# Optimization experiments

Hardware: AMD Instinct MI355X
Metric: run time of the kernel (lower is better)

Reference implementation:

```python
import jax, jax.numpy as jnp
import numpy as np

D_MODEL = 1024
NUM_HEADS = 16
D_FF = 4096
SEQ = 2048
BATCH = 2
THETA = 10000.0
EPS = 1e-5


def _param(key, shape, fan_in, fan_out):
    std = 2.0 / (fan_in + fan_out) ** 0.5
    return std * jax.random.truncated_normal(key, -3.0, 3.0, shape, dtype=jnp.float32)


def setup_inputs() -> dict:
    key = jax.random.key(0)
    ks = jax.random.split(key, 8)
    d, h, f = D_MODEL, NUM_HEADS, D_FF
    return {
        'x': jax.random.normal(ks[0], (BATCH, SEQ, d), dtype=jnp.float32),
        'token_positions': jnp.arange(SEQ, dtype=jnp.int32),
        'wq': _param(ks[1], (d, d), d, d),
        'wk': _param(ks[2], (d, d), d, d),
        'wv': _param(ks[3], (d, d), d, d),
        'wo': _param(ks[4], (d, d), d, d),
        'ln1_w': jnp.ones((d,), jnp.float32),
        'ln2_w': jnp.ones((d,), jnp.float32),
        'w1': _param(ks[5], (f, d), d, f),
        'w2': _param(ks[6], (d, f), f, d),
        'w3': _param(ks[7], (f, d), d, f),
    }


def rmsnorm(x, w):
    x32 = x.astype(jnp.float32)
    rms = jnp.sqrt(jnp.mean(x32 * x32, axis=-1, keepdims=True) + EPS)
    return ((x32 / rms) * w).astype(x.dtype)


def apply_rope(x, cos, sin):
    # x: [b, h, s, d_k]; cos/sin: [s, d_k//2] -> broadcast as [1,1,s,d_k//2]
    xe, xo = x[..., ::2], x[..., 1::2]
    c = cos[None, None, :, :]
    s = sin[None, None, :, :]
    re = xe * c - xo * s
    ro = xe * s + xo * c
    return jnp.stack((re, ro), axis=-1).reshape(x.shape)


def block_forward(x, token_positions, wq, wk, wv, wo, ln1_w, ln2_w, w1, w2, w3):
    b, s, d = x.shape
    h = NUM_HEADS
    dk = d // h
    # RoPE tables at token positions
    inv_freq = 1.0 / (THETA ** (jnp.arange(0, dk // 2, dtype=jnp.float32) * 2.0 / dk))
    freqs = token_positions.astype(jnp.float32)[:, None] * inv_freq[None, :]  # [s, dk/2]
    cos, sin = jnp.cos(freqs), jnp.sin(freqs)

    # --- attention sublayer (pre-norm) ---
    xn = rmsnorm(x, ln1_w)
    q = jnp.einsum('bsd,ed->bse', xn, wq).reshape(b, s, h, dk).transpose(0, 2, 1, 3)
    k = jnp.einsum('bsd,ed->bse', xn, wk).reshape(b, s, h, dk).transpose(0, 2, 1, 3)
    v = jnp.einsum('bsd,ed->bse', xn, wv).reshape(b, s, h, dk).transpose(0, 2, 1, 3)
    q = apply_rope(q, cos, sin)
    k = apply_rope(k, cos, sin)
    scores = jnp.einsum('bhqd,bhkd->bhqk', q, k) / jnp.sqrt(jnp.float32(dk))
    causal = jnp.tril(jnp.ones((s, s), dtype=bool))
    scores = jnp.where(causal[None, None], scores, -jnp.inf)
    attn = jax.nn.softmax(scores, axis=-1)
    o = jnp.einsum('bhqk,bhkd->bhqd', attn, v)
    o = o.transpose(0, 2, 1, 3).reshape(b, s, d)
    x = x + jnp.einsum('bse,de->bsd', o, wo)

    # --- SwiGLU sublayer (pre-norm) ---
    xn = rmsnorm(x, ln2_w)
    x1 = jnp.einsum('bsd,fd->bsf', xn, w1)
    x3 = jnp.einsum('bsd,fd->bsf', xn, w3)
    gated = (x1 * jax.nn.sigmoid(x1)) * x3
    return x + jnp.einsum('bsf,df->bsd', gated, w2)


def reference(x, token_positions, wq, wk, wv, wo, ln1_w, ln2_w, w1, w2, w3):
    return block_forward(x, token_positions, wq, wk, wv, wo, ln1_w, ln2_w, w1, w2, w3)
```

## Files before the change

### kernel.cpp

```cpp
#include <hip/hip_runtime.h>
#include <hip/hip_bf16.h>

typedef __attribute__((ext_vector_type(4))) float f32x4;
typedef __attribute__((ext_vector_type(8))) short bf16x8;
typedef unsigned short u16;
typedef unsigned int u32;
typedef __attribute__((ext_vector_type(4))) u16 u16x4;

#define DEV static __device__ __forceinline__

constexpr int Bb = 2, Ss = 2048, Dd = 1024, Hh = 16, DKk = 64;
constexpr int Mm = Bb * Ss;

DEV float bf2f(u16 u) { union { u32 i; float f; } v; v.i = (u32)u << 16; return v.f; }
DEV u16 f2bf(float f) {
  union { float f; u32 i; } v; v.f = f;
  u32 r = v.i + 0x7FFFu + ((v.i >> 16) & 1u);
  return (u16)(r >> 16);
}

DEV void gload_lds16(const u16* g, u16* l) {
  __builtin_amdgcn_global_load_lds((const __attribute__((address_space(1))) u32*)g,
                                   (__attribute__((address_space(3))) u32*)l, 16, 0, 0);
}

DEV int swz16(int o) {
  return o ^ (((o >> 8) & 1) << 6) ^ (((o >> 9) & 1) << 5);
}

__global__ void k_cvt_all(const float* __restrict__ wq, const float* __restrict__ wk,
                          const float* __restrict__ wv, const float* __restrict__ wo,
                          const float* __restrict__ w1, const float* __restrict__ w2,
                          const float* __restrict__ w3,
                          u16* __restrict__ wqkv, u16* __restrict__ wob,
                          u16* __restrict__ w13, u16* __restrict__ w2b) {
  int i = (blockIdx.x * 256 + threadIdx.x) * 4;
  int seg = i >> 20;
  const float* src; u16* dst;
  if (seg == 0)      { src = wq + i;             dst = wqkv + i; }
  else if (seg == 1) { src = wk + (i - (1<<20)); dst = wqkv + i; }
  else if (seg == 2) { src = wv + (i - (2<<20)); dst = wqkv + i; }
  else if (seg == 3) { src = wo + (i - (3<<20)); dst = wob  + (i - (3<<20)); }
  else if (seg < 8)  { src = w1 + (i - (4<<20)); dst = w13  + (i - (4<<20)); }
  else if (seg < 12) { src = w2 + (i - (8<<20)); dst = w2b  + (i - (8<<20)); }
  else               { src = w3 + (i - (12<<20)); dst = w13 + (4<<20) + (i - (12<<20)); }
  float4 v = *(const float4*)src;
  u16x4 o = { f2bf(v.x), f2bf(v.y), f2bf(v.z), f2bf(v.w) };
  *(u16x4*)dst = o;
}

__global__ __launch_bounds__(256) void k_rmsnorm(const float* __restrict__ x,
                                                 const float* __restrict__ w,
                                                 u16* __restrict__ out) {
  int row = blockIdx.x;
  int t = threadIdx.x;
  float4 v = ((const float4*)(x + (long)row * Dd))[t];
  float ss = v.x * v.x + v.y * v.y + v.z * v.z + v.w * v.w;
#pragma unroll
  for (int m = 32; m; m >>= 1) ss += __shfl_xor(ss, m, 64);
  __shared__ float red[4];
  if ((t & 63) == 0) red[t >> 6] = ss;
  __syncthreads();
  float tot = red[0] + red[1] + red[2] + red[3];
  float r = rsqrtf(tot * (1.0f / Dd) + 1e-5f);
  float4 wv = ((const float4*)w)[t];
  u16x4 o = { f2bf(v.x * r * wv.x), f2bf(v.y * r * wv.y),
              f2bf(v.z * r * wv.z), f2bf(v.w * r * wv.w) };
  ((u16x4*)(out + (long)row * Dd))[t] = o;
}

__global__ void k_rope(u16* __restrict__ q, u16* __restrict__ k, const int* __restrict__ tp) {
  int idx = blockIdx.x * 256 + threadIdx.x;
  if (idx >= Bb * Ss * Hh * 32) return;
  int p = idx & 31;
  int h = (idx >> 5) & 15;
  int row = idx >> 9;
  int s = row & (Ss - 1);
  float pos = (float)tp[s];
  float invf = __expf(-(float)p * (2.0f / DKk) * 9.2103403719761836f);
  float fr = pos * invf;
  float sn, cs;
  sincosf(fr, &sn, &cs);
  long base = (long)row * Dd + h * DKk + 2 * p;
  float xe = bf2f(q[base]), xo = bf2f(q[base + 1]);
  q[base]     = f2bf((xe * cs - xo * sn) * 0.125f);
  q[base + 1] = f2bf((xe * sn + xo * cs) * 0.125f);
  xe = bf2f(k[base]); xo = bf2f(k[base + 1]);
  k[base]     = f2bf(xe * cs - xo * sn);
  k[base + 1] = f2bf(xe * sn + xo * cs);
}

__global__ void k_gate(u16* __restrict__ x1, const u16* __restrict__ x3, int n) {
  int i = (blockIdx.x * 256 + threadIdx.x) * 4;
  if (i >= n) return;
  u16x4 a = *(u16x4*)(x1 + i);
  u16x4 b = *(const u16x4*)(x3 + i);
#pragma unroll
  for (int j = 0; j < 4; j++) {
    float v = bf2f(a[j]);
    float g = v / (1.0f + __expf(-v)) * bf2f(b[j]);
    a[j] = f2bf(g);
  }
  *(u16x4*)(x1 + i) = a;
}

__global__ void k_addout(const float* __restrict__ p0, const float* __restrict__ p1,
                         const float* __restrict__ x2, float* __restrict__ out) {
  int i = (blockIdx.x * 256 + threadIdx.x) * 4;
  float4 a = *(const float4*)(p0 + i);
  float4 b = *(const float4*)(p1 + i);
  float4 c = *(const float4*)(x2 + i);
  float4 o = { a.x + b.x + c.x, a.y + b.y + c.y, a.z + b.z + c.z, a.w + b.w + c.w };
  *(float4*)(out + i) = o;
}

template <int OM, bool RES>
__global__ __launch_bounds__(256) void k_gemm(const u16* __restrict__ A,
                                              const u16* __restrict__ Bm,
                                              void* __restrict__ Cout,
                                              const float* __restrict__ Rres,
                                              int N, int Kl, int Kstr) {
  __shared__ u16 Abuf[128 * 32];
  __shared__ u16 Bbuf[128 * 32];
  const int tid = threadIdx.x;
  const int wid = tid >> 6, lane = tid & 63;
  const int wm = wid >> 1, wn = wid & 1;
  const int lq = lane >> 4, ll = lane & 15;
  const int lin = blockIdx.y * gridDim.x + blockIdx.x;
  const int c = lin & 7, j = lin >> 3;
  const int ncc = gridDim.x >> 2;
  const int bxc = (c % ncc) * 4 + (j & 3);
  const int byc = (c / ncc) * 8 + (j >> 2);
  const int m0 = byc * 128, n0 = bxc * 128;

  const u16* Ap = A + (long)blockIdx.z * Kl;
  const u16* Bp = Bm + (long)blockIdx.z * Kl;

  f32x4 acc[4][4] = {};

  const int srow = tid >> 2;
  const int scol = (tid & 3) * 8;
  const long aoff = (long)(m0 + srow) * Kstr + scol;
  const long boff = (long)(n0 + srow) * Kstr + scol;
  u16* aldsw = Abuf + wid * 512;
  u16* bldsw = Bbuf + wid * 512;

  for (int k0 = 0; k0 < Kl; k0 += 32) {
    __syncthreads();
    gload_lds16(Ap + aoff + k0, aldsw);
    gload_lds16(Ap + aoff + (long)64 * Kstr + k0, aldsw + 2048);
    gload_lds16(Bp + boff + k0, bldsw);
    gload_lds16(Bp + boff + (long)64 * Kstr + k0, bldsw + 2048);
    __syncthreads();
    bf16x8 af[4], bfr[4];
#pragma unroll
    for (int i = 0; i < 4; i++)
      af[i] = *(const bf16x8*)&Abuf[(wm * 64 + i * 16 + ll) * 32 + lq * 8];
#pragma unroll
    for (int j2 = 0; j2 < 4; j2++)
      bfr[j2] = *(const bf16x8*)&Bbuf[(wn * 64 + j2 * 16 + ll) * 32 + lq * 8];
#pragma unroll
    for (int i = 0; i < 4; i++)
#pragma unroll
      for (int j2 = 0; j2 < 4; j2++)
        acc[i][j2] = __builtin_amdgcn_mfma_f32_16x16x32_bf16(af[i], bfr[j2], acc[i][j2], 0, 0, 0);
  }

  float* fout = (float*)Cout + (long)blockIdx.z * Mm * (long)N;
#pragma unroll
  for (int i = 0; i < 4; i++) {
    const int rowb = m0 + wm * 64 + i * 16 + lq * 4;
#pragma unroll
    for (int j2 = 0; j2 < 4; j2++) {
      const int col = n0 + wn * 64 + j2 * 16 + ll;
#pragma unroll
      for (int r = 0; r < 4; r++) {
        int rr = rowb + r;
        float v = acc[i][j2][r];
        if (RES) v += Rres[(long)rr * N + col];
        if (OM == 1) {
          fout[(long)rr * N + col] = v;
        } else {
          ((u16*)Cout)[(long)rr * N + col] = f2bf(v);
        }
      }
    }
  }
}

#define STG_A(d, h, kt)                                                         \
  { gload_lds16(A + aoff[0] + (long)(h) * 128 * K + (kt) * 64, &sA[d][h][dst0]); \
    gload_lds16(A + aoff[1] + (long)(h) * 128 * K + (kt) * 64, &sA[d][h][dst1]); }
#define STG_B(d, h, kt)                                                         \
  { gload_lds16(Bm + boff[0] + (long)(h) * 128 * K + (kt) * 64, &sB[d][h][dst0]); \
    gload_lds16(Bm + boff[1] + (long)(h) * 128 * K + (kt) * 64, &sB[d][h][dst1]); }

#define PHASE(q, d, DOB, WVN, ...)                                              \
  {                                                                             \
    bf16x8 af_[2][2];                                                           \
    _Pragma("unroll") for (int s_ = 0; s_ < 2; s_++)                            \
    _Pragma("unroll") for (int kk_ = 0; kk_ < 2; kk_++) {                       \
      int ms_ = (q) * 4 + wm * 2 + s_;                                          \
      int lo_ = ((ms_ & 7) * 16 + ll) * 128 + kk_ * 64 + lq * 16;               \
      af_[s_][kk_] = *(const bf16x8*)((const char*)sA[d][ms_ >> 3] + swz16(lo_)); \
    }                                                                           \
    if (DOB) {                                                                  \
      _Pragma("unroll") for (int ns_ = 0; ns_ < 4; ns_++)                       \
      _Pragma("unroll") for (int kk_ = 0; kk_ < 2; kk_++) {                     \
        int rl_ = wn * 64 + ns_ * 16 + ll;                                      \
        int lo_ = (rl_ & 127) * 128 + kk_ * 64 + lq * 16;                       \
        bfr[ns_][kk_] = *(const bf16x8*)((const char*)sB[d][rl_ >> 7] + swz16(lo_)); \
      }                                                                         \
    }                                                                           \
    __VA_ARGS__;                                                                \
    __builtin_amdgcn_s_barrier();                                               \
    asm volatile("s_waitcnt lgkmcnt(0)" ::: "memory");                          \
    __builtin_amdgcn_sched_barrier(0);                                          \
    __builtin_amdgcn_s_setprio(1);                                              \
    _Pragma("unroll") for (int s_ = 0; s_ < 2; s_++)                            \
    _Pragma("unroll") for (int ns_ = 0; ns_ < 4; ns_++)                         \
    _Pragma("unroll") for (int kk_ = 0; kk_ < 2; kk_++)                         \
      acc[q][s_][ns_] = __builtin_amdgcn_mfma_f32_16x16x32_bf16(                \
          af_[s_][kk_], bfr[ns_][kk_], acc[q][s_][ns_], 0, 0, 0);               \
    __builtin_amdgcn_s_setprio(0);                                              \
    { int wv_ = (WVN);                                                          \
      if (wv_ == 6) { asm volatile("s_waitcnt vmcnt(6)" ::: "memory"); }        \
      else if (wv_ == 0) { asm volatile("s_waitcnt vmcnt(0)" ::: "memory"); } } \
    __builtin_amdgcn_s_barrier();                                               \
  }

template <int OM, int CW, int CH>
__global__ __launch_bounds__(512) void k_gemm8(const u16* __restrict__ A,
                                               const u16* __restrict__ Bm,
                                               void* __restrict__ Cout,
                                               int N, int K) {
  __shared__ u16 sA[2][2][8192];
  __shared__ u16 sB[2][2][8192];
  const int gx = gridDim.x;
  const int lin = blockIdx.y * gx + blockIdx.x;
  const int c = lin & 7, j = lin >> 3;
  const int ncc = gx / CW;
  const int bx = (c % ncc) * CW + j % CW;
  const int by = (c / ncc) * CH + j / CW;
  const long m0 = (long)by * 256, n0 = (long)bx * 256;
  const int tid = threadIdx.x;
  const int wid = tid >> 6, lane = tid & 63;
  const int wm = wid >> 2, wn = wid & 3;
  const int lq = lane >> 4, ll = lane & 15;

  long aoff[2], boff[2];
#pragma unroll
  for (int j2 = 0; j2 < 2; j2++) {
    int off = j2 * 8192 + wid * 1024 + lane * 16;
    int lo = swz16(off);
    int r = lo >> 7, cc = (lo & 127) >> 1;
    aoff[j2] = (m0 + r) * K + cc;
    boff[j2] = (n0 + r) * K + cc;
  }
  const int dst0 = wid * 512;
  const int dst1 = 4096 + wid * 512;

  f32x4 acc[4][2][4] = {};
  bf16x8 bfr[4][2];

  const int NT = K >> 6;
  const int NI = NT >> 1;

  STG_A(0, 0, 0); STG_A(0, 1, 0); STG_B(0, 0, 0); STG_B(0, 1, 0);
  STG_B(1, 0, 1); STG_B(1, 1, 1); STG_A(1, 0, 1);
  asm volatile("s_waitcnt vmcnt(6)" ::: "memory");
  __builtin_amdgcn_s_barrier();

  for (int it = 0; it < NI; it++) {
    const int t = 2 * it;
    const bool full = (t + 2 < NT);
    PHASE(0, 0, true,  -1,            STG_A(1, 1, t + 1))
    PHASE(1, 0, false, -1,            if (full) STG_B(0, 0, t + 2))
    PHASE(2, 0, false, -1,            if (full) STG_B(0, 1, t + 2))
    PHASE(3, 0, false, full ? 6 : 0,  if (full) STG_A(0, 0, t + 2))
    PHASE(0, 1, true,  -1,            if (full) STG_A(0, 1, t + 2))
    PHASE(1, 1, false, -1,            if (full) STG_B(1, 0, t + 3))
    PHASE(2, 1, false, -1,            if (full) STG_B(1, 1, t + 3))
    PHASE(3, 1, false, full ? 6 : -1, if (full) STG_A(1, 0, t + 3))
  }

#pragma unroll
  for (int q = 0; q < 4; q++)
#pragma unroll
    for (int s = 0; s < 2; s++) {
      const long row0 = m0 + (q * 4 + wm * 2 + s) * 16 + lq * 4;
#pragma unroll
      for (int ns = 0; ns < 4; ns++) {
        const long col = n0 + wn * 64 + ns * 16 + ll;
#pragma unroll
        for (int r = 0; r < 4; r++) {
          float v = acc[q][s][ns][r];
          long rr = row0 + r;
          if (OM == 3) {
            if (col < 2048) {
              ((u16*)Cout)[(col >> 10) * (long)(Mm * 1024) + rr * 1024 + (col & 1023)] = f2bf(v);
            } else {
              int d = col & 63, hh = ((int)col >> 6) & 15;
              int b2 = (int)rr >> 11, s2 = (int)rr & (Ss - 1);
              ((u16*)Cout)[(long)(2 * Mm * 1024) + ((long)((b2 * Hh + hh) * DKk + d)) * Ss + s2] = f2bf(v);
            }
          } else {
            ((u16*)Cout)[(col >> 12) * ((long)Mm * 4096) + rr * 4096 + (col & 4095)] = f2bf(v);
          }
        }
      }
    }
}

constexpr int PPAD = 80;

DEV void attn_tile(const u16* __restrict__ Kc, const u16* __restrict__ Vc,
                   u16* __restrict__ myP, const bf16x8* qf, f32x4* accO,
                   float* mrow, float* lrow, int qloc, bool diag, int lq, int ll) {
  f32x4 sacc[4] = {};
#pragma unroll
  for (int fn = 0; fn < 4; fn++)
#pragma unroll
    for (int ks = 0; ks < 2; ks++) {
      bf16x8 kf = *(const bf16x8*)&Kc[(fn * 16 + ll) * 64 + (((ks * 4 + lq) ^ (ll & 7)) * 8)];
      sacc[fn] = __builtin_amdgcn_mfma_f32_16x16x32_bf16(qf[ks], kf, sacc[fn], 0, 0, 0);
    }
  float sv[4][4], pmax[4];
#pragma unroll
  for (int r = 0; r < 4; r++) pmax[r] = -1e30f;
#pragma unroll
  for (int fn = 0; fn < 4; fn++) {
    int kc = fn * 16 + ll;
#pragma unroll
    for (int r = 0; r < 4; r++) {
      float v = sacc[fn][r];
      if (diag && kc > qloc + r) v = -1e30f;
      sv[fn][r] = v;
      pmax[r] = fmaxf(pmax[r], v);
    }
  }
#pragma unroll
  for (int r = 0; r < 4; r++) {
#pragma unroll
    for (int m = 1; m < 16; m <<= 1) pmax[r] = fmaxf(pmax[r], __shfl_xor(pmax[r], m, 64));
  }
  float alpha[4], rsum[4];
#pragma unroll
  for (int r = 0; r < 4; r++) {
    float mnew = fmaxf(mrow[r], pmax[r]);
    alpha[r] = __expf(mrow[r] - mnew);
    mrow[r] = mnew;
    rsum[r] = 0.f;
  }
#pragma unroll
  for (int fn = 0; fn < 4; fn++) {
#pragma unroll
    for (int r = 0; r < 4; r++) {
      float p = __expf(sv[fn][r] - mrow[r]);
      rsum[r] += p;
      myP[(lq * 4 + r) * PPAD + fn * 16 + ll] = f2bf(p);
    }
  }
#pragma unroll
  for (int r = 0; r < 4; r++) {
#pragma unroll
    for (int m = 1; m < 16; m <<= 1) rsum[r] += __shfl_xor(rsum[r], m, 64);
    lrow[r] = lrow[r] * alpha[r] + rsum[r];
  }
#pragma unroll
  for (int fn = 0; fn < 4; fn++)
#pragma unroll
    for (int r = 0; r < 4; r++) accO[fn][r] *= alpha[r];
  bf16x8 pa[2];
#pragma unroll
  for (int ks = 0; ks < 2; ks++)
    pa[ks] = *(const bf16x8*)&myP[ll * PPAD + ks * 32 + lq * 8];
#pragma unroll
  for (int fn = 0; fn < 4; fn++)
#pragma unroll
    for (int ks = 0; ks < 2; ks++) {
      bf16x8 vf = *(const bf16x8*)&Vc[(fn * 16 + ll) * 64 + (((ks * 4 + lq) ^ (ll & 7)) * 8)];
      accO[fn] = __builtin_amdgcn_mfma_f32_16x16x32_bf16(pa[ks], vf, accO[fn], 0, 0, 0);
    }
}

__global__ __launch_bounds__(256) void k_attn(const u16* __restrict__ Q,
                                              const u16* __restrict__ Kb,
                                              const u16* __restrict__ VT,
                                              u16* __restrict__ O) {
  __shared__ u16 Kt[2][64 * 64];
  __shared__ u16 Vt[2][64 * 64];
  __shared__ u16 P[4][16 * PPAD];
  const int pair = blockIdx.x;
  const int bh = blockIdx.y;
  const int b = bh >> 4, h = bh & 15;
  const int tid = threadIdx.x;
  const int wid = tid >> 6, lane = tid & 63;
  const int lq = lane >> 4, ll = lane & 15;
  const int qtA = pair, qtB = 31 - pair;
  const int qr0A = qtA * 64 + wid * 16;
  const int qr0B = qtB * 64 + wid * 16;
  const int qloc = wid * 16 + lq * 4;
  const long qkbase = ((long)b * Ss) * Dd + h * DKk;
  const long vbase  = ((long)(b * Hh + h) * DKk) * Ss;
  const int nk = 32 - pair;

  const int slot0 = wid * 64 + lane;
  const int r0 = slot0 >> 3, c0 = (slot0 & 7) ^ (r0 & 7);
  const int slot1 = 256 + slot0;
  const int r1 = slot1 >> 3, c1 = (slot1 & 7) ^ (r1 & 7);
  const int ldsb0 = (wid * 64) * 8;
  const int ldsb1 = (256 + wid * 64) * 8;

  bf16x8 qfA[2], qfB[2];
#pragma unroll
  for (int ks = 0; ks < 2; ks++) {
    qfA[ks] = *(const bf16x8*)&Q[qkbase + (long)(qr0A + ll) * Dd + ks * 32 + lq * 8];
    qfB[ks] = *(const bf16x8*)&Q[qkbase + (long)(qr0B + ll) * Dd + ks * 32 + lq * 8];
  }

  f32x4 accA[4] = {}, accB[4] = {};
  float mA[4], lA[4], mB[4], lB[4];
#pragma unroll
  for (int r = 0; r < 4; r++) { mA[r] = mB[r] = -1e30f; lA[r] = lB[r] = 0.f; }
  u16* myP = P[wid];

  gload_lds16(Kb + qkbase + (long)r0 * Dd + c0 * 8, Kt[0] + ldsb0);
  gload_lds16(Kb + qkbase + (long)r1 * Dd + c1 * 8, Kt[0] + ldsb1);
  gload_lds16(VT + vbase + (long)r0 * Ss + c0 * 8, Vt[0] + ldsb0);
  gload_lds16(VT + vbase + (long)r1 * Ss + c1 * 8, Vt[0] + ldsb1);
  __syncthreads();

  for (int kt = 0; kt < nk; kt++) {
    if (kt + 1 < nk) {
      const int kn = (kt + 1) * 64;
      u16* kd = Kt[(kt + 1) & 1];
      u16* vd = Vt[(kt + 1) & 1];
      gload_lds16(Kb + qkbase + (long)(kn + r0) * Dd + c0 * 8, kd + ldsb0);
      gload_lds16(Kb + qkbase + (long)(kn + r1) * Dd + c1 * 8, kd + ldsb1);
      gload_lds16(VT + vbase + (long)r0 * Ss + kn + c0 * 8, vd + ldsb0);
      gload_lds16(VT + vbase + (long)r1 * Ss + kn + c1 * 8, vd + ldsb1);
    }
    const u16* Kc = Kt[kt & 1];
    const u16* Vc = Vt[kt & 1];

    attn_tile(Kc, Vc, myP, qfB, accB, mB, lB, qloc, kt == nk - 1, lq, ll);
    if (kt <= pair)
      attn_tile(Kc, Vc, myP, qfA, accA, mA, lA, qloc, kt == pair, lq, ll);
    __syncthreads();
  }

#pragma unroll
  for (int fn = 0; fn < 4; fn++) {
#pragma unroll
    for (int r = 0; r < 4; r++) {
      int rowA = qr0A + lq * 4 + r;
      int rowB = qr0B + lq * 4 + r;
      O[((long)(b * Ss + rowA)) * Dd + h * DKk + fn * 16 + ll] = f2bf(accA[fn][r] / lA[r]);
      O[((long)(b * Ss + rowB)) * Dd + h * DKk + fn * 16 + ll] = f2bf(accB[fn][r] / lB[r]);
    }
  }
}

extern "C" void kernel_launch(void* const* d_in, const int* in_sizes, int n_in,
                              void* d_out, int out_size, void* d_ws, size_t ws_size,
                              hipStream_t stream) {
  const float* x   = (const float*)d_in[0];
  const int*   tp  = (const int*)d_in[1];
  const float* wq  = (const float*)d_in[2];
  const float* wk  = (const float*)d_in[3];
  const float* wv  = (const float*)d_in[4];
  const float* wo  = (const float*)d_in[5];
  const float* ln1 = (const float*)d_in[6];
  const float* ln2 = (const float*)d_in[7];
  const float* w1  = (const float*)d_in[8];
  const float* w2  = (const float*)d_in[9];
  const float* w3  = (const float*)d_in[10];

  char* ws = (char*)d_ws;
  const size_t MB = 1024 * 1024;
  u16*   wqkv_b = (u16*)(ws + 0 * MB);
  u16*   wo_b   = (u16*)(ws + 6 * MB);
  u16*   w13_b  = (u16*)(ws + 8 * MB);
  u16*   w2_b   = (u16*)(ws + 24 * MB);
  u16*   xn     = (u16*)(ws + 32 * MB);
  float* x2     = (float*)(ws + 40 * MB);
  u16*   qb     = (u16*)(ws + 56 * MB);
  u16*   kb     = (u16*)(ws + 64 * MB);
  u16*   vtb    = (u16*)(ws + 72 * MB);
  u16*   ob     = (u16*)(ws + 80 * MB);
  u16*   x1     = (u16*)(ws + 56 * MB);
  u16*   x3     = (u16*)(ws + 88 * MB);
  float* p0     = (float*)(ws + 88 * MB);
  float* p1     = (float*)(ws + 104 * MB);

  k_cvt_all<<<16384, 256, 0, stream>>>(wq, wk, wv, wo, w1, w2, w3,
                                       wqkv_b, wo_b, w13_b, w2_b);
  k_rmsnorm<<<Mm, 256, 0, stream>>>(x, ln1, xn);
  k_gemm8<3, 6, 4><<<dim3(12, 16), 512, 0, stream>>>(xn, wqkv_b, qb, 3072, 1024);
  k_rope<<<(Bb * Ss * Hh * 32) / 256, 256, 0, stream>>>(qb, kb, tp);
  k_attn<<<dim3(16, 32), 256, 0, stream>>>(qb, kb, vtb, ob);
  k_gemm<1, true><<<dim3(8, 32), 256, 0, stream>>>(ob, wo_b, x2, x, 1024, 1024, 1024);
  k_rmsnorm<<<Mm, 256, 0, stream>>>(x2, ln2, xn);
  k_gemm8<4, 4, 8><<<dim3(32, 16), 512, 0, stream>>>(xn, w13_b, x1, 8192, 1024);
  k_gate<<<16384, 256, 0, stream>>>(x1, x3, 4096 * 4096);
  k_gemm<1, false><<<dim3(8, 32, 2), 256, 0, stream>>>(x1, w2_b, p0, nullptr, 1024, 2048, 4096);
  k_addout<<<4096, 256, 0, stream>>>(p0, p1, x2, (float*)d_out);
}
```

Before: 357.5 us.

## Fuse SwiGLU gate into W1/W3 GEMM epilogue and raise MFMA priority in attention

The W1/W3 GEMM now computes both the x1 and x3 tiles in the same workgroup, running two passes over K. It stashes the first result in global memory as bf16 and applies SiLU gating in the second pass's epilogue, which removes the separate gate kernel and one full write and read of an intermediate. The attention MFMA sections are also wrapped in s_setprio to favour matrix issue. In exchange, the grid for that GEMM is halved, the A tile is loaded twice per block, and the stash round-trip still costs global traffic.

```diff
diff --git a/kernel.cpp b/kernel.cpp
--- a/kernel.cpp
+++ b/kernel.cpp
@@ -90,20 +90,6 @@
   k[base + 1] = f2bf(xe * sn + xo * cs);
 }
 
-__global__ void k_gate(u16* __restrict__ x1, const u16* __restrict__ x3, int n) {
-  int i = (blockIdx.x * 256 + threadIdx.x) * 4;
-  if (i >= n) return;
-  u16x4 a = *(u16x4*)(x1 + i);
-  u16x4 b = *(const u16x4*)(x3 + i);
-#pragma unroll
-  for (int j = 0; j < 4; j++) {
-    float v = bf2f(a[j]);
-    float g = v / (1.0f + __expf(-v)) * bf2f(b[j]);
-    a[j] = f2bf(g);
-  }
-  *(u16x4*)(x1 + i) = a;
-}
-
 __global__ void k_addout(const float* __restrict__ p0, const float* __restrict__ p1,
                          const float* __restrict__ x2, float* __restrict__ out) {
   int i = (blockIdx.x * 256 + threadIdx.x) * 4;
@@ -192,8 +178,8 @@
   { gload_lds16(A + aoff[0] + (long)(h) * 128 * K + (kt) * 64, &sA[d][h][dst0]); \
     gload_lds16(A + aoff[1] + (long)(h) * 128 * K + (kt) * 64, &sA[d][h][dst1]); }
 #define STG_B(d, h, kt)                                                         \
-  { gload_lds16(Bm + boff[0] + (long)(h) * 128 * K + (kt) * 64, &sB[d][h][dst0]); \
-    gload_lds16(Bm + boff[1] + (long)(h) * 128 * K + (kt) * 64, &sB[d][h][dst1]); }
+  { gload_lds16(Bp + boff[0] + (long)(h) * 128 * K + (kt) * 64, &sB[d][h][dst0]); \
+    gload_lds16(Bp + boff[1] + (long)(h) * 128 * K + (kt) * 64, &sB[d][h][dst1]); }
 
 #define PHASE(q, d, DOB, WVN, ...)                                              \
   {                                                                             \
@@ -233,6 +219,7 @@
 __global__ __launch_bounds__(512) void k_gemm8(const u16* __restrict__ A,
                                                const u16* __restrict__ Bm,
                                                void* __restrict__ Cout,
+                                               u16* __restrict__ gstash,
                                                int N, int K) {
   __shared__ u16 sA[2][2][8192];
   __shared__ u16 sB[2][2][8192];
@@ -260,28 +247,56 @@
   const int dst0 = wid * 512;
   const int dst1 = 4096 + wid * 512;
 
-  f32x4 acc[4][2][4] = {};
+  f32x4 acc[4][2][4];
   bf16x8 bfr[4][2];
 
   const int NT = K >> 6;
   const int NI = NT >> 1;
-
-  STG_A(0, 0, 0); STG_A(0, 1, 0); STG_B(0, 0, 0); STG_B(0, 1, 0);
-  STG_B(1, 0, 1); STG_B(1, 1, 1); STG_A(1, 0, 1);
-  asm volatile("s_waitcnt vmcnt(6)" ::: "memory");
-  __builtin_amdgcn_s_barrier();
-
-  for (int it = 0; it < NI; it++) {
-    const int t = 2 * it;
-    const bool full = (t + 2 < NT);
-    PHASE(0, 0, true,  -1,            STG_A(1, 1, t + 1))
-    PHASE(1, 0, false, -1,            if (full) STG_B(0, 0, t + 2))
-    PHASE(2, 0, false, -1,            if (full) STG_B(0, 1, t + 2))
-    PHASE(3, 0, false, full ? 6 : 0,  if (full) STG_A(0, 0, t + 2))
-    PHASE(0, 1, true,  -1,            if (full) STG_A(0, 1, t + 2))
-    PHASE(1, 1, false, -1,            if (full) STG_B(1, 0, t + 3))
-    PHASE(2, 1, false, -1,            if (full) STG_B(1, 1, t + 3))
-    PHASE(3, 1, false, full ? 6 : -1, if (full) STG_A(1, 0, t + 3))
+  constexpr int REPS = (OM == 5) ? 2 : 1;
+
+  for (int rep = 0; rep < REPS; rep++) {
+    const u16* Bp = Bm + (long)rep * 4096 * K;
+    const f32x4 zz = {0.f, 0.f, 0.f, 0.f};
+#pragma unroll
+    for (int q = 0; q < 4; q++)
+#pragma unroll
+      for (int s = 0; s < 2; s++)
+#pragma unroll
+        for (int ns = 0; ns < 4; ns++) acc[q][s][ns] = zz;
+
+    STG_A(0, 0, 0); STG_A(0, 1, 0); STG_B(0, 0, 0); STG_B(0, 1, 0);
+    STG_B(1, 0, 1); STG_B(1, 1, 1); STG_A(1, 0, 1);
+    asm volatile("s_waitcnt vmcnt(6)" ::: "memory");
+    __builtin_amdgcn_s_barrier();
+
+    for (int it = 0; it < NI; it++) {
+      const int t = 2 * it;
+      const bool full = (t + 2 < NT);
+      PHASE(0, 0, true,  -1,            STG_A(1, 1, t + 1))
+      PHASE(1, 0, false, -1,            if (full) STG_B(0, 0, t + 2))
+      PHASE(2, 0, false, -1,            if (full) STG_B(0, 1, t + 2))
+      PHASE(3, 0, false, full ? 6 : 0,  if (full) STG_A(0, 0, t + 2))
+      PHASE(0, 1, true,  -1,            if (full) STG_A(0, 1, t + 2))
+      PHASE(1, 1, false, -1,            if (full) STG_B(1, 0, t + 3))
+      PHASE(2, 1, false, -1,            if (full) STG_B(1, 1, t + 3))
+      PHASE(3, 1, false, full ? 6 : -1, if (full) STG_A(1, 0, t + 3))
+    }
+
+    if (OM == 5 && rep == 0) {
+#pragma unroll
+      for (int q = 0; q < 4; q++)
+#pragma unroll
+        for (int s = 0; s < 2; s++) {
+          const long row0 = m0 + (q * 4 + wm * 2 + s) * 16 + lq * 4;
+#pragma unroll
+          for (int ns = 0; ns < 4; ns++) {
+            const long col = n0 + wn * 64 + ns * 16 + ll;
+#pragma unroll
+            for (int r = 0; r < 4; r++)
+              gstash[(row0 + r) * 4096 + col] = f2bf(acc[q][s][ns][r]);
+          }
+        }
+    }
   }
 
 #pragma unroll
@@ -305,7 +320,9 @@
               ((u16*)Cout)[(long)(2 * Mm * 1024) + ((long)((b2 * Hh + hh) * DKk + d)) * Ss + s2] = f2bf(v);
             }
           } else {
-            ((u16*)Cout)[(col >> 12) * ((long)Mm * 4096) + rr * 4096 + (col & 4095)] = f2bf(v);
+            float v1 = bf2f(gstash[rr * 4096 + col]);
+            float g = v1 / (1.0f + __expf(-v1)) * v;
+            ((u16*)Cout)[rr * 4096 + col] = f2bf(g);
           }
         }
       }
@@ -318,6 +335,7 @@
                    u16* __restrict__ myP, const bf16x8* qf, f32x4* accO,
                    float* mrow, float* lrow, int qloc, bool diag, int lq, int ll) {
   f32x4 sacc[4] = {};
+  __builtin_amdgcn_s_setprio(1);
 #pragma unroll
   for (int fn = 0; fn < 4; fn++)
 #pragma unroll
@@ -325,6 +343,7 @@
       bf16x8 kf = *(const bf16x8*)&Kc[(fn * 16 + ll) * 64 + (((ks * 4 + lq) ^ (ll & 7)) * 8)];
       sacc[fn] = __builtin_amdgcn_mfma_f32_16x16x32_bf16(qf[ks], kf, sacc[fn], 0, 0, 0);
     }
+  __builtin_amdgcn_s_setprio(0);
   float sv[4][4], pmax[4];
 #pragma unroll
   for (int r = 0; r < 4; r++) pmax[r] = -1e30f;
@@ -375,6 +394,7 @@
 #pragma unroll
   for (int ks = 0; ks < 2; ks++)
     pa[ks] = *(const bf16x8*)&myP[ll * PPAD + ks * 32 + lq * 8];
+  __builtin_amdgcn_s_setprio(1);
 #pragma unroll
   for (int fn = 0; fn < 4; fn++)
 #pragma unroll
@@ -382,6 +402,7 @@
       bf16x8 vf = *(const bf16x8*)&Vc[(fn * 16 + ll) * 64 + (((ks * 4 + lq) ^ (ll & 7)) * 8)];
       accO[fn] = __builtin_amdgcn_mfma_f32_16x16x32_bf16(pa[ks], vf, accO[fn], 0, 0, 0);
     }
+  __builtin_amdgcn_s_setprio(0);
 }
 
 __global__ __launch_bounds__(256) void k_attn(const u16* __restrict__ Q,
@@ -490,20 +511,19 @@
   u16*   vtb    = (u16*)(ws + 72 * MB);
   u16*   ob     = (u16*)(ws + 80 * MB);
   u16*   x1     = (u16*)(ws + 56 * MB);
-  u16*   x3     = (u16*)(ws + 88 * MB);
+  u16*   stash  = (u16*)(ws + 88 * MB);
   float* p0     = (float*)(ws + 88 * MB);
   float* p1     = (float*)(ws + 104 * MB);
 
   k_cvt_all<<<16384, 256, 0, stream>>>(wq, wk, wv, wo, w1, w2, w3,
                                        wqkv_b, wo_b, w13_b, w2_b);
   k_rmsnorm<<<Mm, 256, 0, stream>>>(x, ln1, xn);
-  k_gemm8<3, 6, 4><<<dim3(12, 16), 512, 0, stream>>>(xn, wqkv_b, qb, 3072, 1024);
+  k_gemm8<3, 6, 4><<<dim3(12, 16), 512, 0, stream>>>(xn, wqkv_b, qb, nullptr, 3072, 1024);
   k_rope<<<(Bb * Ss * Hh * 32) / 256, 256, 0, stream>>>(qb, kb, tp);
   k_attn<<<dim3(16, 32), 256, 0, stream>>>(qb, kb, vtb, ob);
   k_gemm<1, true><<<dim3(8, 32), 256, 0, stream>>>(ob, wo_b, x2, x, 1024, 1024, 1024);
   k_rmsnorm<<<Mm, 256, 0, stream>>>(x2, ln2, xn);
-  k_gemm8<4, 4, 8><<<dim3(32, 16), 512, 0, stream>>>(xn, w13_b, x1, 8192, 1024);
-  k_gate<<<16384, 256, 0, stream>>>(x1, x3, 4096 * 4096);
+  k_gemm8<5, 4, 8><<<dim3(16, 16), 512, 0, stream>>>(xn, w13_b, x1, stash, 4096, 1024);
   k_gemm<1, false><<<dim3(8, 32, 2), 256, 0, stream>>>(x1, w2_b, p0, nullptr, 1024, 2048, 4096);
   k_addout<<<4096, 256, 0, stream>>>(p0, p1, x2, (float*)d_out);
 }
```

After: 468.6 us. +31.1%, slower.
